# Optimization experiments

Hardware: AMD Instinct MI355X
Metric: run time of the kernel (lower is better)

The kernel has to match this reference:

```python
import jax, jax.numpy as jnp
import numpy as np

B, S, E, H = 2, 2048, 1024, 16
D = E // H  # head_dim = 64


def setup_inputs() -> dict:
    key = jax.random.key(0)
    ks = jax.random.split(key, 6)
    scale = 1.0 / np.sqrt(E)
    query = jax.random.normal(ks[0], (B, S, E), dtype=jnp.float32)
    key_t = jax.random.normal(ks[1], (B, S, E), dtype=jnp.float32)
    # causal mask: True where future positions should be masked
    attention_mask = jnp.triu(jnp.ones((S, S), dtype=jnp.bool_), k=1)
    wq = jax.random.normal(ks[2], (E, E), dtype=jnp.float32) * scale
    wk = jax.random.normal(ks[3], (E, E), dtype=jnp.float32) * scale
    wv = jax.random.normal(ks[4], (E, E), dtype=jnp.float32) * scale
    wo = jax.random.normal(ks[5], (E, E), dtype=jnp.float32) * scale
    return {"query": query, "key": key_t, "attention_mask": attention_mask,
            "wq": wq, "wk": wk, "wv": wv, "wo": wo}


def _split_heads(x):
    # (B, S, E) -> (B, H, S, D)
    return x.reshape(B, S, H, D).transpose(0, 2, 1, 3)


def reference(query, key, attention_mask, wq, wk, wv, wo):
    # self-attention (encoder_decoder_attention=False): k, v from query
    q = _split_heads(query @ wq.T)
    k = _split_heads(query @ wk.T)
    v = _split_heads(query @ wv.T)
    scores = jnp.einsum('bhqd,bhkd->bhqk', q, k) / np.sqrt(D)
    # causal mask broadcast (1,1,S,S)
    scores = jnp.where(attention_mask[None, None, :, :], -jnp.inf, scores)
    attn_weights = jax.nn.softmax(scores, axis=-1)
    # drop_out = 0.0, so dropout is identity
    attn_out = jnp.einsum('bhqk,bhkd->bhqd', attn_weights, v)
    attn_out = attn_out.transpose(0, 2, 1, 3).reshape(B, S, E)
    attn_out = attn_out @ wo.T
    return attn_out, attn_weights
```

## Files before the change

kernel.cpp:

```cpp
#include <hip/hip_runtime.h>
#include <hip/hip_bf16.h>
#include <cstdint>

#define S_LEN 2048
#define EMB 1024
#define NHEAD 16
#define HDIM 64
#define NB 2
#define MTOT (NB * S_LEN)

typedef __attribute__((ext_vector_type(8))) __bf16 bf16x8;
typedef __attribute__((ext_vector_type(8))) unsigned short us8;
typedef __attribute__((ext_vector_type(4))) unsigned short us4;
typedef __attribute__((ext_vector_type(4))) float f32x4;

__device__ __forceinline__ unsigned short f2b(float f) {
  unsigned int u = __float_as_uint(f);
  u = (u + 0x7FFFu + ((u >> 16) & 1u)) >> 16;
  return (unsigned short)u;
}
__device__ __forceinline__ unsigned short f2b_tr(float f) {
  return (unsigned short)(__float_as_uint(f) >> 16);
}
__device__ __forceinline__ float b2f(unsigned short u) {
  return __uint_as_float((unsigned int)u << 16);
}
__device__ __forceinline__ bf16x8 ld8(const unsigned short* p) {
  return __builtin_bit_cast(bf16x8, *(const us8*)p);
}
__device__ __forceinline__ void gload16(const void* g, void* l) {
  __builtin_amdgcn_global_load_lds(
      (const __attribute__((address_space(1))) unsigned int*)g,
      (__attribute__((address_space(3))) unsigned int*)l, 16, 0, 0);
}
__device__ __forceinline__ void st_nt(float* p, f32x4 v) {
  __builtin_nontemporal_store(v, (f32x4*)p);
}
__device__ __forceinline__ void bar_lds() {
  asm volatile("s_waitcnt lgkmcnt(0)" ::: "memory");
  __builtin_amdgcn_sched_barrier(0);
  __builtin_amdgcn_s_barrier();
}
__device__ __forceinline__ void fence_lds_wave() {
  asm volatile("s_waitcnt lgkmcnt(0)" ::: "memory");
  __builtin_amdgcn_sched_barrier(0);
}

__global__ void conv_fused(const float* __restrict__ X,
                           const float* __restrict__ wq, const float* __restrict__ wk,
                           const float* __restrict__ wv, const float* __restrict__ wo,
                           unsigned short* __restrict__ xb,
                           unsigned short* __restrict__ wb) {
  int i = blockIdx.x * blockDim.x + threadIdx.x;
  const float* s;
  unsigned short* o;
  int j;
  float sc = 1.0f;
  if (i < MTOT * EMB / 4) {
    s = X; j = i; o = xb;
  } else {
    int k = i - MTOT * EMB / 4;
    int sel = k >> 18;
    j = k & 262143;
    s = sel == 0 ? wq : sel == 1 ? wk : sel == 2 ? wv : wo;
    o = wb + (size_t)sel * EMB * EMB;
    if (sel == 0) sc = 0.125f;
  }
  float4 v = reinterpret_cast<const float4*>(s)[j];
  us4 ov;
  ov[0] = f2b(v.x * sc); ov[1] = f2b(v.y * sc);
  ov[2] = f2b(v.z * sc); ov[3] = f2b(v.w * sc);
  reinterpret_cast<us4*>(o)[j] = ov;
}

__global__ __launch_bounds__(256)
void vtrans(const unsigned short* __restrict__ V, unsigned short* __restrict__ VT) {
  __shared__ unsigned short Vs[64][72];
  const int s0 = blockIdx.x * 64;
  const int bh = blockIdx.y, b = bh >> 4, h = bh & 15;
  const unsigned short* Vb = V + (size_t)b * S_LEN * EMB + h * HDIM;
  const int t = threadIdx.x;
  {
    int row = t >> 2, c0 = (t & 3) * 16;
    const unsigned short* src = Vb + (size_t)(s0 + row) * EMB + c0;
    *(us8*)&Vs[row][c0] = *(const us8*)src;
    *(us8*)&Vs[row][c0 + 8] = *(const us8*)(src + 8);
  }
  __syncthreads();
  int d = t >> 2, sc = (t & 3) * 16;
  us8 o0, o1;
#pragma unroll
  for (int j = 0; j < 8; ++j) { o0[j] = Vs[sc + j][d]; o1[j] = Vs[sc + 8 + j][d]; }
  unsigned short* dst = VT + ((size_t)bh * HDIM + d) * S_LEN + s0 + sc;
  *(us8*)dst = o0;
  *(us8*)(dst + 8) = o1;
}

template <typename OT>
__global__ __launch_bounds__(256)
void gemm_bt(const unsigned short* __restrict__ A,
             const unsigned short* __restrict__ Wb,
             OT* __restrict__ Cb) {
  __shared__ unsigned short As[128 * 32];
  __shared__ unsigned short Bs[128 * 32];
  const int t = threadIdx.x;
  const int w = t >> 6, l = t & 63;
  const int m0 = blockIdx.x * 128;
  const int n0g = blockIdx.y * 128;
  const int wsel = n0g >> 10;
  const int n0 = n0g & 1023;
  const unsigned short* W = Wb + (size_t)wsel * ((size_t)EMB * EMB);
  OT* C = Cb + (size_t)wsel * ((size_t)MTOT * EMB);
  const int wr = (w >> 1) * 64, wc = (w & 1) * 64;
  const int fr = l & 15, fk = (l >> 4) * 8;
  const f32x4 fz = {0.f, 0.f, 0.f, 0.f};
  f32x4 acc[4][4];
  for (int i = 0; i < 4; i++)
    for (int j = 0; j < 4; j++) acc[i][j] = fz;
  const int srow = t >> 2, scol = (t & 3) * 8;
  const unsigned short* Ar = A + (size_t)(m0 + srow) * EMB + scol;
  const unsigned short* Wr = W + (size_t)(n0 + srow) * EMB + scol;
  unsigned short* lA = &As[t * 8];
  unsigned short* lB = &Bs[t * 8];
  for (int k0 = 0; k0 < EMB; k0 += 32) {
    gload16(Ar + k0, lA);
    gload16(Ar + (size_t)64 * EMB + k0, lA + 64 * 32);
    gload16(Wr + k0, lB);
    gload16(Wr + (size_t)64 * EMB + k0, lB + 64 * 32);
    __syncthreads();
    bf16x8 af[4], bg[4];
#pragma unroll
    for (int i = 0; i < 4; i++) {
      af[i] = ld8(&As[(wr + i * 16 + fr) * 32 + fk]);
      bg[i] = ld8(&Bs[(wc + i * 16 + fr) * 32 + fk]);
    }
#pragma unroll
    for (int i = 0; i < 4; i++)
#pragma unroll
      for (int j = 0; j < 4; j++)
        acc[i][j] = __builtin_amdgcn_mfma_f32_16x16x32_bf16(af[i], bg[j], acc[i][j], 0, 0, 0);
    __syncthreads();
  }
  const int cr = (l >> 4) * 4, cc = l & 15;
#pragma unroll
  for (int i = 0; i < 4; i++)
#pragma unroll
    for (int j = 0; j < 4; j++) {
      int m = m0 + wr + i * 16 + cr;
      int n = n0 + wc + j * 16 + cc;
      OT* dst = C + (size_t)m * EMB + n;
#pragma unroll
      for (int r = 0; r < 4; r++) {
        if constexpr (sizeof(OT) == 2)
          dst[(size_t)r * EMB] = f2b(acc[i][j][r]);
        else
          __builtin_nontemporal_store(acc[i][j][r], dst + (size_t)r * EMB);
      }
    }
}

__global__ __launch_bounds__(256, 3)
void attn_fwd(const unsigned short* __restrict__ Q,
              const unsigned short* __restrict__ K,
              const unsigned short* __restrict__ VT,
              unsigned short* __restrict__ AO,
              float* __restrict__ WT) {
  __shared__ __align__(16) unsigned char smem[9216 * 4];
  unsigned short* Ks  = (unsigned short*)smem;
  unsigned short* Vt  = (unsigned short*)(smem + 9216);
  unsigned short* PsA = (unsigned short*)(smem + 18432);
  unsigned short* PsB = (unsigned short*)(smem + 27648);
  unsigned short* QsA = PsA;
  unsigned short* QsB = PsB;
  unsigned short* OlA = PsA;
  unsigned short* OlB = PsB;

  const int t = threadIdx.x, w = t >> 6, l = t & 63;
  const int bh = blockIdx.x, b = bh >> 4, h = bh & 15;
  const int p = blockIdx.y;
  const int qA = p, qB = (S_LEN / 64 - 1) - p;
  const int ntA = qA + 1, ntB = qB + 1;
  const unsigned short* Qb = Q + (size_t)b * S_LEN * EMB + h * HDIM;
  const unsigned short* Kb = K + (size_t)b * S_LEN * EMB + h * HDIM;
  const unsigned short* VTb = VT + (size_t)bh * HDIM * S_LEN;
  const int fr = l & 15, fk = (l >> 4) * 8;
  const int rg = (l >> 4) * 4;
  const int qrowA = qA * 64 + w * 16 + rg;
  const int qrowB = qB * 64 + w * 16 + rg;
  const f32x4 fz = {0.f, 0.f, 0.f, 0.f};
  const int srow = t >> 3, scol = (t & 7) * 8;
  const int zrow = l >> 4, zcol = (l & 15) * 4;

  {
    int row = t >> 2, c0 = (t & 3) * 16;
    const unsigned short* sA = Qb + (size_t)(qA * 64 + row) * EMB + c0;
    const unsigned short* sB = Qb + (size_t)(qB * 64 + row) * EMB + c0;
    *(us8*)&QsA[row * 72 + c0] = *(const us8*)sA;
    *(us8*)&QsA[row * 72 + c0 + 8] = *(const us8*)(sA + 8);
    *(us8*)&QsB[row * 72 + c0] = *(const us8*)sB;
    *(us8*)&QsB[row * 72 + c0 + 8] = *(const us8*)(sB + 8);
  }
  __syncthreads();
  bf16x8 qaA0 = ld8(&QsA[(w * 16 + fr) * 72 + fk]);
  bf16x8 qaA1 = ld8(&QsA[(w * 16 + fr) * 72 + 32 + fk]);
  bf16x8 qaB0 = ld8(&QsB[(w * 16 + fr) * 72 + fk]);
  bf16x8 qaB1 = ld8(&QsB[(w * 16 + fr) * 72 + 32 + fk]);

  float lrA[4], lrB[4];
#pragma unroll
  for (int r = 0; r < 4; r++) { lrA[r] = 0.f; lrB[r] = 0.f; }

  us8 k0r = *(const us8*)(Kb + (size_t)srow * EMB + scol);
  us8 k1r = *(const us8*)(Kb + (size_t)(srow + 32) * EMB + scol);
  for (int it = 0; it < ntB; ++it) {
    *(us8*)&Ks[srow * 72 + scol] = k0r;
    *(us8*)&Ks[(srow + 32) * 72 + scol] = k1r;
    us8 k0n, k1n;
    if (it + 1 < ntB) {
      const unsigned short* kn = Kb + (size_t)((it + 1) * 64) * EMB;
      k0n = *(const us8*)(kn + (size_t)srow * EMB + scol);
      k1n = *(const us8*)(kn + (size_t)(srow + 32) * EMB + scol);
    }
    bar_lds();
    const int kc = it * 64;
    const bool doA = (it < ntA);
    const bool diagA = (it == ntA - 1), diagB = (it == ntB - 1);
#pragma unroll
    for (int c = 0; c < 4; ++c) {
      bf16x8 kb0 = ld8(&Ks[(c * 16 + fr) * 72 + fk]);
      bf16x8 kb1 = ld8(&Ks[(c * 16 + fr) * 72 + 32 + fk]);
      int ki = kc + c * 16 + fr;
      if (doA) {
        f32x4 dd = fz;
        dd = __builtin_amdgcn_mfma_f32_16x16x32_bf16(qaA0, kb0, dd, 0, 0, 0);
        dd = __builtin_amdgcn_mfma_f32_16x16x32_bf16(qaA1, kb1, dd, 0, 0, 0);
#pragma unroll
        for (int r = 0; r < 4; ++r) {
          float e = __expf(dd[r]);
          if (diagA && ki > qrowA + r) e = 0.f;
          lrA[r] += e;
        }
      }
      {
        f32x4 dd = fz;
        dd = __builtin_amdgcn_mfma_f32_16x16x32_bf16(qaB0, kb0, dd, 0, 0, 0);
        dd = __builtin_amdgcn_mfma_f32_16x16x32_bf16(qaB1, kb1, dd, 0, 0, 0);
#pragma unroll
        for (int r = 0; r < 4; ++r) {
          float e = __expf(dd[r]);
          if (diagB && ki > qrowB + r) e = 0.f;
          lrB[r] += e;
        }
      }
    }
    if (!doA) {
#pragma unroll
      for (int s4 = 0; s4 < 4; ++s4) {
        int rowl = s4 * 4 + zrow;
        st_nt(&WT[((size_t)bh * S_LEN + qA * 64 + w * 16 + rowl) * S_LEN + kc + zcol], fz);
      }
    }
    bar_lds();
    k0r = k0n; k1r = k1n;
  }
  for (int it = ntB; it < 32; ++it) {
    const int kc = it * 64;
#pragma unroll
    for (int s4 = 0; s4 < 4; ++s4) {
      int rowl = s4 * 4 + zrow;
      size_t rbase = (size_t)bh * S_LEN;
      st_nt(&WT[(rbase + qA * 64 + w * 16 + rowl) * S_LEN + kc + zcol], fz);
      st_nt(&WT[(rbase + qB * 64 + w * 16 + rowl) * S_LEN + kc + zcol], fz);
    }
  }
#pragma unroll
  for (int r = 0; r < 4; ++r) {
    float lA = lrA[r], lB = lrB[r];
    for (int s = 1; s < 16; s <<= 1) {
      lA += __shfl_xor(lA, s, 64);
      lB += __shfl_xor(lB, s, 64);
    }
    lrA[r] = 1.0f / lA;
    lrB[r] = 1.0f / lB;
  }

  f32x4 accA[4], accB[4];
#pragma unroll
  for (int i = 0; i < 4; i++) { accA[i] = fz; accB[i] = fz; }
  unsigned short* PsAw = PsA + w * (16 * 72);
  unsigned short* PsBw = PsB + w * (16 * 72);
  us8 v0r, v1r;
  k0r = *(const us8*)(Kb + (size_t)srow * EMB + scol);
  k1r = *(const us8*)(Kb + (size_t)(srow + 32) * EMB + scol);
  v0r = *(const us8*)(VTb + (size_t)srow * S_LEN + scol);
  v1r = *(const us8*)(VTb + (size_t)(srow + 32) * S_LEN + scol);
  for (int it = 0; it < ntB; ++it) {
    *(us8*)&Ks[srow * 72 + scol] = k0r;
    *(us8*)&Ks[(srow + 32) * 72 + scol] = k1r;
    *(us8*)&Vt[srow * 72 + scol] = v0r;
    *(us8*)&Vt[(srow + 32) * 72 + scol] = v1r;
    us8 k0n, k1n, v0n, v1n;
    if (it + 1 < ntB) {
      const int kc1 = (it + 1) * 64;
      const unsigned short* kn = Kb + (size_t)kc1 * EMB;
      k0n = *(const us8*)(kn + (size_t)srow * EMB + scol);
      k1n = *(const us8*)(kn + (size_t)(srow + 32) * EMB + scol);
      v0n = *(const us8*)(VTb + (size_t)srow * S_LEN + kc1 + scol);
      v1n = *(const us8*)(VTb + (size_t)(srow + 32) * S_LEN + kc1 + scol);
    }
    bar_lds();
    const int kc = it * 64;
    const bool doA = (it < ntA);
    const bool diagA = (it == ntA - 1), diagB = (it == ntB - 1);
#pragma unroll
    for (int c = 0; c < 4; ++c) {
      bf16x8 kb0 = ld8(&Ks[(c * 16 + fr) * 72 + fk]);
      bf16x8 kb1 = ld8(&Ks[(c * 16 + fr) * 72 + 32 + fk]);
      int ki = kc + c * 16 + fr;
      if (doA) {
        f32x4 dd = fz;
        dd = __builtin_amdgcn_mfma_f32_16x16x32_bf16(qaA0, kb0, dd, 0, 0, 0);
        dd = __builtin_amdgcn_mfma_f32_16x16x32_bf16(qaA1, kb1, dd, 0, 0, 0);
#pragma unroll
        for (int r = 0; r < 4; ++r) {
          float e = __expf(dd[r]);
          if (diagA && ki > qrowA + r) e = 0.f;
          PsAw[(rg + r) * 72 + c * 16 + fr] = f2b_tr(e * lrA[r]);
        }
      }
      {
        f32x4 dd = fz;
        dd = __builtin_amdgcn_mfma_f32_16x16x32_bf16(qaB0, kb0, dd, 0, 0, 0);
        dd = __builtin_amdgcn_mfma_f32_16x16x32_bf16(qaB1, kb1, dd, 0, 0, 0);
#pragma unroll
        for (int r = 0; r < 4; ++r) {
          float e = __expf(dd[r]);
          if (diagB && ki > qrowB + r) e = 0.f;
          PsBw[(rg + r) * 72 + c * 16 + fr] = f2b_tr(e * lrB[r]);
        }
      }
    }
    fence_lds_wave();
#pragma unroll
    for (int ks = 0; ks < 2; ++ks) {
      bf16x8 paA, paB;
      if (doA) paA = ld8(&PsAw[fr * 72 + ks * 32 + fk]);
      paB = ld8(&PsBw[fr * 72 + ks * 32 + fk]);
#pragma unroll
      for (int dt = 0; dt < 4; ++dt) {
        bf16x8 vb = ld8(&Vt[(dt * 16 + fr) * 72 + ks * 32 + fk]);
        if (doA) accA[dt] = __builtin_amdgcn_mfma_f32_16x16x32_bf16(paA, vb, accA[dt], 0, 0, 0);
        accB[dt] = __builtin_amdgcn_mfma_f32_16x16x32_bf16(paB, vb, accB[dt], 0, 0, 0);
      }
    }
    if (doA) {
#pragma unroll
      for (int s4 = 0; s4 < 4; ++s4) {
        int rowl = s4 * 4 + zrow;
        us4 pv = *(const us4*)&PsAw[rowl * 72 + zcol];
        f32x4 v;
#pragma unroll
        for (int j = 0; j < 4; ++j) v[j] = b2f(pv[j]);
        st_nt(&WT[((size_t)bh * S_LEN + qA * 64 + w * 16 + rowl) * S_LEN + kc + zcol], v);
      }
    }
#pragma unroll
    for (int s4 = 0; s4 < 4; ++s4) {
      int rowl = s4 * 4 + zrow;
      us4 pv = *(const us4*)&PsBw[rowl * 72 + zcol];
      f32x4 v;
#pragma unroll
      for (int j = 0; j < 4; ++j) v[j] = b2f(pv[j]);
      st_nt(&WT[((size_t)bh * S_LEN + qB * 64 + w * 16 + rowl) * S_LEN + kc + zcol], v);
    }
    bar_lds();
    k0r = k0n; k1r = k1n; v0r = v0n; v1r = v1n;
  }

#pragma unroll
  for (int dt = 0; dt < 4; ++dt)
#pragma unroll
    for (int r = 0; r < 4; ++r) {
      OlA[(w * 16 + rg + r) * 72 + dt * 16 + fr] = f2b(accA[dt][r]);
      OlB[(w * 16 + rg + r) * 72 + dt * 16 + fr] = f2b(accB[dt][r]);
    }
  __syncthreads();
  {
    int rowl = l >> 2, d0 = (l & 3) * 16;
    us8 a0 = *(const us8*)&OlA[(w * 16 + rowl) * 72 + d0];
    us8 a1 = *(const us8*)&OlA[(w * 16 + rowl) * 72 + d0 + 8];
    unsigned short* dA = AO + (size_t)(b * S_LEN + qA * 64 + w * 16 + rowl) * EMB + h * HDIM + d0;
    *(us8*)dA = a0;
    *(us8*)(dA + 8) = a1;
    us8 b0 = *(const us8*)&OlB[(w * 16 + rowl) * 72 + d0];
    us8 b1 = *(const us8*)&OlB[(w * 16 + rowl) * 72 + d0 + 8];
    unsigned short* dB = AO + (size_t)(b * S_LEN + qB * 64 + w * 16 + rowl) * EMB + h * HDIM + d0;
    *(us8*)dB = b0;
    *(us8*)(dB + 8) = b1;
  }
}

extern "C" void kernel_launch(void* const* d_in, const int* in_sizes, int n_in,
                              void* d_out, int out_size, void* d_ws, size_t ws_size,
                              hipStream_t stream) {
  const float* query = (const float*)d_in[0];
  const float* wq = (const float*)d_in[3];
  const float* wk = (const float*)d_in[4];
  const float* wv = (const float*)d_in[5];
  const float* wo = (const float*)d_in[6];

  float* out0 = (float*)d_out;
  float* wout = out0 + (size_t)MTOT * EMB;

  unsigned short* xb  = (unsigned short*)d_ws;
  unsigned short* wqb = xb + (size_t)MTOT * EMB;
  unsigned short* wob = wqb + (size_t)3 * EMB * EMB;
  unsigned short* qb  = wqb + (size_t)4 * EMB * EMB;
  unsigned short* kb  = qb + (size_t)MTOT * EMB;
  unsigned short* vb  = kb + (size_t)MTOT * EMB;
  unsigned short* ab  = vb + (size_t)MTOT * EMB;
  unsigned short* vtg = xb;

  conv_fused<<<dim3(8192), dim3(256), 0, stream>>>(query, wq, wk, wv, wo, xb, wqb);

  gemm_bt<unsigned short><<<dim3(MTOT / 128, 24), dim3(256), 0, stream>>>(xb, wqb, qb);

  vtrans<<<dim3(S_LEN / 64, NB * NHEAD), dim3(256), 0, stream>>>(vb, vtg);

  attn_fwd<<<dim3(NB * NHEAD, S_LEN / 128), dim3(256), 0, stream>>>(qb, kb, vtg, ab, wout);

  gemm_bt<float><<<dim3(MTOT / 128, 8), dim3(256), 0, stream>>>(ab, wob, out0);
}
```

Measured before the change: 226.8 us.

## Split attention work so each wave owns one query tile half, doubling grid

Each block now handles 32 query rows from tile A and 32 from tile B. Waves 0-1 handle tile A and waves 2-3 handle tile B, instead of every wave computing both tiles. The grid doubles with a z dimension, LDS shrinks from 36 KiB to 27 KiB, and launch bounds rise to 4 blocks per CU, all to raise occupancy and cut per-thread register pressure from the dual accumulators. In exchange, each K/V tile loaded into LDS now serves only 32 rows per tile, so K/V traffic doubles. Waves for the short tile also idle while the long-tile waves iterate.

Result: slower. 245.7 us (+8.3%).

```diff
diff --git a/kernel.cpp b/kernel.cpp
--- a/kernel.cpp
+++ b/kernel.cpp
@@ -159,56 +159,53 @@
     }
 }
 
-__global__ __launch_bounds__(256, 3)
+__global__ __launch_bounds__(256, 4)
 void attn_fwd(const unsigned short* __restrict__ Q,
               const unsigned short* __restrict__ K,
               const unsigned short* __restrict__ VT,
               unsigned short* __restrict__ AO,
               float* __restrict__ WT) {
-  __shared__ __align__(16) unsigned char smem[9216 * 4];
+  __shared__ __align__(16) unsigned char smem[27648];
   unsigned short* Ks  = (unsigned short*)smem;
   unsigned short* Vt  = (unsigned short*)(smem + 9216);
   unsigned short* PsA = (unsigned short*)(smem + 18432);
-  unsigned short* PsB = (unsigned short*)(smem + 27648);
-  unsigned short* QsA = PsA;
-  unsigned short* QsB = PsB;
-  unsigned short* OlA = PsA;
-  unsigned short* OlB = PsB;
+  unsigned short* PsB = (unsigned short*)(smem + 23040);
 
   const int t = threadIdx.x, w = t >> 6, l = t & 63;
-  const int bh = blockIdx.x, b = bh >> 4, h = bh & 15;
-  const int p = blockIdx.y;
-  const int qA = p, qB = (S_LEN / 64 - 1) - p;
-  const int ntA = qA + 1, ntB = qB + 1;
+  const int p = blockIdx.x;
+  const int bh = blockIdx.y, b = bh >> 4, h = bh & 15;
+  const int z = blockIdx.z;
+  const int qA = p, qB = 31 - p;
+  const int ntA = p + 1, ntB = 32 - p;
+  const int half = w >> 1;
+  const int wrow = (w & 1) * 16;
+  const int nt = half ? ntB : ntA;
+  const int qbase = (half ? qB : qA) * 64 + z * 32;
   const unsigned short* Qb = Q + (size_t)b * S_LEN * EMB + h * HDIM;
   const unsigned short* Kb = K + (size_t)b * S_LEN * EMB + h * HDIM;
   const unsigned short* VTb = VT + (size_t)bh * HDIM * S_LEN;
   const int fr = l & 15, fk = (l >> 4) * 8;
   const int rg = (l >> 4) * 4;
-  const int qrowA = qA * 64 + w * 16 + rg;
-  const int qrowB = qB * 64 + w * 16 + rg;
+  const int qrow = qbase + wrow + rg;
   const f32x4 fz = {0.f, 0.f, 0.f, 0.f};
   const int srow = t >> 3, scol = (t & 7) * 8;
   const int zrow = l >> 4, zcol = (l & 15) * 4;
+  unsigned short* Psh = half ? PsB : PsA;
 
   {
-    int row = t >> 2, c0 = (t & 3) * 16;
-    const unsigned short* sA = Qb + (size_t)(qA * 64 + row) * EMB + c0;
-    const unsigned short* sB = Qb + (size_t)(qB * 64 + row) * EMB + c0;
-    *(us8*)&QsA[row * 72 + c0] = *(const us8*)sA;
-    *(us8*)&QsA[row * 72 + c0 + 8] = *(const us8*)(sA + 8);
-    *(us8*)&QsB[row * 72 + c0] = *(const us8*)sB;
-    *(us8*)&QsB[row * 72 + c0 + 8] = *(const us8*)(sB + 8);
+    int row = t >> 3, c0 = (t & 7) * 8;
+    *(us8*)&PsA[row * 72 + c0] =
+        *(const us8*)(Qb + (size_t)(qA * 64 + z * 32 + row) * EMB + c0);
+    *(us8*)&PsB[row * 72 + c0] =
+        *(const us8*)(Qb + (size_t)(qB * 64 + z * 32 + row) * EMB + c0);
   }
   __syncthreads();
-  bf16x8 qaA0 = ld8(&QsA[(w * 16 + fr) * 72 + fk]);
-  bf16x8 qaA1 = ld8(&QsA[(w * 16 + fr) * 72 + 32 + fk]);
-  bf16x8 qaB0 = ld8(&QsB[(w * 16 + fr) * 72 + fk]);
-  bf16x8 qaB1 = ld8(&QsB[(w * 16 + fr) * 72 + 32 + fk]);
-
-  float lrA[4], lrB[4];
-#pragma unroll
-  for (int r = 0; r < 4; r++) { lrA[r] = 0.f; lrB[r] = 0.f; }
+  bf16x8 qa0 = ld8(&Psh[(wrow + fr) * 72 + fk]);
+  bf16x8 qa1 = ld8(&Psh[(wrow + fr) * 72 + 32 + fk]);
+
+  float lr[4];
+#pragma unroll
+  for (int r = 0; r < 4; r++) lr[r] = 0.f;
 
   us8 k0r = *(const us8*)(Kb + (size_t)srow * EMB + scol);
   us8 k1r = *(const us8*)(Kb + (size_t)(srow + 32) * EMB + scol);
@@ -223,41 +220,28 @@
     }
     bar_lds();
     const int kc = it * 64;
-    const bool doA = (it < ntA);
-    const bool diagA = (it == ntA - 1), diagB = (it == ntB - 1);
-#pragma unroll
-    for (int c = 0; c < 4; ++c) {
-      bf16x8 kb0 = ld8(&Ks[(c * 16 + fr) * 72 + fk]);
-      bf16x8 kb1 = ld8(&Ks[(c * 16 + fr) * 72 + 32 + fk]);
-      int ki = kc + c * 16 + fr;
-      if (doA) {
+    if (it < nt) {
+      const bool diag = (it == nt - 1);
+#pragma unroll
+      for (int c = 0; c < 4; ++c) {
+        bf16x8 kb0 = ld8(&Ks[(c * 16 + fr) * 72 + fk]);
+        bf16x8 kb1 = ld8(&Ks[(c * 16 + fr) * 72 + 32 + fk]);
         f32x4 dd = fz;
-        dd = __builtin_amdgcn_mfma_f32_16x16x32_bf16(qaA0, kb0, dd, 0, 0, 0);
-        dd = __builtin_amdgcn_mfma_f32_16x16x32_bf16(qaA1, kb1, dd, 0, 0, 0);
+        dd = __builtin_amdgcn_mfma_f32_16x16x32_bf16(qa0, kb0, dd, 0, 0, 0);
+        dd = __builtin_amdgcn_mfma_f32_16x16x32_bf16(qa1, kb1, dd, 0, 0, 0);
+        int ki = kc + c * 16 + fr;
 #pragma unroll
         for (int r = 0; r < 4; ++r) {
           float e = __expf(dd[r]);
-          if (diagA && ki > qrowA + r) e = 0.f;
-          lrA[r] += e;
+          if (diag && ki > qrow + r) e = 0.f;
+          lr[r] += e;
         }
       }
-      {
-        f32x4 dd = fz;
-        dd = __builtin_amdgcn_mfma_f32_16x16x32_bf16(qaB0, kb0, dd, 0, 0, 0);
-        dd = __builtin_amdgcn_mfma_f32_16x16x32_bf16(qaB1, kb1, dd, 0, 0, 0);
-#pragma unroll
-        for (int r = 0; r < 4; ++r) {
-          float e = __expf(dd[r]);
-          if (diagB && ki > qrowB + r) e = 0.f;
-          lrB[r] += e;
-        }
-      }
-    }
-    if (!doA) {
+    } else {
 #pragma unroll
       for (int s4 = 0; s4 < 4; ++s4) {
         int rowl = s4 * 4 + zrow;
-        st_nt(&WT[((size_t)bh * S_LEN + qA * 64 + w * 16 + rowl) * S_LEN + kc + zcol], fz);
+        st_nt(&WT[((size_t)bh * S_LEN + qbase + wrow + rowl) * S_LEN + kc + zcol], fz);
       }
     }
     bar_lds();
@@ -268,27 +252,19 @@
 #pragma unroll
     for (int s4 = 0; s4 < 4; ++s4) {
       int rowl = s4 * 4 + zrow;
-      size_t rbase = (size_t)bh * S_LEN;
-      st_nt(&WT[(rbase + qA * 64 + w * 16 + rowl) * S_LEN + kc + zcol], fz);
-      st_nt(&WT[(rbase + qB * 64 + w * 16 + rowl) * S_LEN + kc + zcol], fz);
+      st_nt(&WT[((size_t)bh * S_LEN + qbase + wrow + rowl) * S_LEN + kc + zcol], fz);
     }
   }
 #pragma unroll
   for (int r = 0; r < 4; ++r) {
-    float lA = lrA[r], lB = lrB[r];
-    for (int s = 1; s < 16; s <<= 1) {
-      lA += __shfl_xor(lA, s, 64);
-      lB += __shfl_xor(lB, s, 64);
-    }
-    lrA[r] = 1.0f / lA;
-    lrB[r] = 1.0f / lB;
-  }
-
-  f32x4 accA[4], accB[4];
-#pragma unroll
-  for (int i = 0; i < 4; i++) { accA[i] = fz; accB[i] = fz; }
-  unsigned short* PsAw = PsA + w * (16 * 72);
-  unsigned short* PsBw = PsB + w * (16 * 72);
+    float v = lr[r];
+    for (int s = 1; s < 16; s <<= 1) v += __shfl_xor(v, s, 64);
+    lr[r] = 1.0f / v;
+  }
+
+  f32x4 acc[4];
+#pragma unroll
+  for (int i = 0; i < 4; i++) acc[i] = fz;
   us8 v0r, v1r;
   k0r = *(const us8*)(Kb + (size_t)srow * EMB + scol);
   k1r = *(const us8*)(Kb + (size_t)(srow + 32) * EMB + scol);
@@ -310,68 +286,42 @@
     }
     bar_lds();
     const int kc = it * 64;
-    const bool doA = (it < ntA);
-    const bool diagA = (it == ntA - 1), diagB = (it == ntB - 1);
-#pragma unroll
-    for (int c = 0; c < 4; ++c) {
-      bf16x8 kb0 = ld8(&Ks[(c * 16 + fr) * 72 + fk]);
-      bf16x8 kb1 = ld8(&Ks[(c * 16 + fr) * 72 + 32 + fk]);
-      int ki = kc + c * 16 + fr;
-      if (doA) {
+    if (it < nt) {
+      const bool diag = (it == nt - 1);
+#pragma unroll
+      for (int c = 0; c < 4; ++c) {
+        bf16x8 kb0 = ld8(&Ks[(c * 16 + fr) * 72 + fk]);
+        bf16x8 kb1 = ld8(&Ks[(c * 16 + fr) * 72 + 32 + fk]);
         f32x4 dd = fz;
-        dd = __builtin_amdgcn_mfma_f32_16x16x32_bf16(qaA0, kb0, dd, 0, 0, 0);
-        dd = __builtin_amdgcn_mfma_f32_16x16x32_bf16(qaA1, kb1, dd, 0, 0, 0);
+        dd = __builtin_amdgcn_mfma_f32_16x16x32_bf16(qa0, kb0, dd, 0, 0, 0);
+        dd = __builtin_amdgcn_mfma_f32_16x16x32_bf16(qa1, kb1, dd, 0, 0, 0);
+        int ki = kc + c * 16 + fr;
 #pragma unroll
         for (int r = 0; r < 4; ++r) {
           float e = __expf(dd[r]);
-          if (diagA && ki > qrowA + r) e = 0.f;
-          PsAw[(rg + r) * 72 + c * 16 + fr] = f2b_tr(e * lrA[r]);
+          if (diag && ki > qrow + r) e = 0.f;
+          Psh[(wrow + rg + r) * 72 + c * 16 + fr] = f2b_tr(e * lr[r]);
         }
       }
-      {
-        f32x4 dd = fz;
-        dd = __builtin_amdgcn_mfma_f32_16x16x32_bf16(qaB0, kb0, dd, 0, 0, 0);
-        dd = __builtin_amdgcn_mfma_f32_16x16x32_bf16(qaB1, kb1, dd, 0, 0, 0);
-#pragma unroll
-        for (int r = 0; r < 4; ++r) {
-          float e = __expf(dd[r]);
-          if (diagB && ki > qrowB + r) e = 0.f;
-          PsBw[(rg + r) * 72 + c * 16 + fr] = f2b_tr(e * lrB[r]);
+      fence_lds_wave();
+#pragma unroll
+      for (int ks = 0; ks < 2; ++ks) {
+        bf16x8 pa = ld8(&Psh[(wrow + fr) * 72 + ks * 32 + fk]);
+#pragma unroll
+        for (int dt = 0; dt < 4; ++dt) {
+          bf16x8 vb = ld8(&Vt[(dt * 16 + fr) * 72 + ks * 32 + fk]);
+          acc[dt] = __builtin_amdgcn_mfma_f32_16x16x32_bf16(pa, vb, acc[dt], 0, 0, 0);
         }
       }
-    }
-    fence_lds_wave();
-#pragma unroll
-    for (int ks = 0; ks < 2; ++ks) {
-      bf16x8 paA, paB;
-      if (doA) paA = ld8(&PsAw[fr * 72 + ks * 32 + fk]);
-      paB = ld8(&PsBw[fr * 72 + ks * 32 + fk]);
-#pragma unroll
-      for (int dt = 0; dt < 4; ++dt) {
-        bf16x8 vb = ld8(&Vt[(dt * 16 + fr) * 72 + ks * 32 + fk]);
-        if (doA) accA[dt] = __builtin_amdgcn_mfma_f32_16x16x32_bf16(paA, vb, accA[dt], 0, 0, 0);
-        accB[dt] = __builtin_amdgcn_mfma_f32_16x16x32_bf16(paB, vb, accB[dt], 0, 0, 0);
-      }
-    }
-    if (doA) {
 #pragma unroll
       for (int s4 = 0; s4 < 4; ++s4) {
         int rowl = s4 * 4 + zrow;
-        us4 pv = *(const us4*)&PsAw[rowl * 72 + zcol];
+        us4 pv = *(const us4*)&Psh[(wrow + rowl) * 72 + zcol];
         f32x4 v;
 #pragma unroll
         for (int j = 0; j < 4; ++j) v[j] = b2f(pv[j]);
-        st_nt(&WT[((size_t)bh * S_LEN + qA * 64 + w * 16 + rowl) * S_LEN + kc + zcol], v);
-      }
-    }
-#pragma unroll
-    for (int s4 = 0; s4 < 4; ++s4) {
-      int rowl = s4 * 4 + zrow;
-      us4 pv = *(const us4*)&PsBw[rowl * 72 + zcol];
-      f32x4 v;
-#pragma unroll
-      for (int j = 0; j < 4; ++j) v[j] = b2f(pv[j]);
-      st_nt(&WT[((size_t)bh * S_LEN + qB * 64 + w * 16 + rowl) * S_LEN + kc + zcol], v);
+        st_nt(&WT[((size_t)bh * S_LEN + qbase + wrow + rowl) * S_LEN + kc + zcol], v);
+      }
     }
     bar_lds();
     k0r = k0n; k1r = k1n; v0r = v0n; v1r = v1n;
@@ -380,23 +330,21 @@
 #pragma unroll
   for (int dt = 0; dt < 4; ++dt)
 #pragma unroll
-    for (int r = 0; r < 4; ++r) {
-      OlA[(w * 16 + rg + r) * 72 + dt * 16 + fr] = f2b(accA[dt][r]);
-      OlB[(w * 16 + rg + r) * 72 + dt * 16 + fr] = f2b(accB[dt][r]);
-    }
+    for (int r = 0; r < 4; ++r)
+      Psh[(wrow + rg + r) * 72 + dt * 16 + fr] = f2b(acc[dt][r]);
   __syncthreads();
   {
-    int rowl = l >> 2, d0 = (l & 3) * 16;
-    us8 a0 = *(const us8*)&OlA[(w * 16 + rowl) * 72 + d0];
-    us8 a1 = *(const us8*)&OlA[(w * 16 + rowl) * 72 + d0 + 8];
-    unsigned short* dA = AO + (size_t)(b * S_LEN + qA * 64 + w * 16 + rowl) * EMB + h * HDIM + d0;
-    *(us8*)dA = a0;
-    *(us8*)(dA + 8) = a1;
-    us8 b0 = *(const us8*)&OlB[(w * 16 + rowl) * 72 + d0];
-    us8 b1 = *(const us8*)&OlB[(w * 16 + rowl) * 72 + d0 + 8];
-    unsigned short* dB = AO + (size_t)(b * S_LEN + qB * 64 + w * 16 + rowl) * EMB + h * HDIM + d0;
-    *(us8*)dB = b0;
-    *(us8*)(dB + 8) = b1;
+    int orow = t >> 2;
+    int oh = orow >> 5, orl = orow & 31;
+    int d0 = (t & 3) * 16;
+    const unsigned short* osrc =
+        (const unsigned short*)(smem + 18432 + oh * 4608) + orl * 72 + d0;
+    us8 o0 = *(const us8*)osrc;
+    us8 o1 = *(const us8*)(osrc + 8);
+    int grow = (oh ? qB : qA) * 64 + z * 32 + orl;
+    unsigned short* dst = AO + (size_t)(b * S_LEN + grow) * EMB + h * HDIM + d0;
+    *(us8*)dst = o0;
+    *(us8*)(dst + 8) = o1;
   }
 }
 
@@ -427,7 +375,7 @@
 
   vtrans<<<dim3(S_LEN / 64, NB * NHEAD), dim3(256), 0, stream>>>(vb, vtg);
 
-  attn_fwd<<<dim3(NB * NHEAD, S_LEN / 128), dim3(256), 0, stream>>>(qb, kb, vtg, ab, wout);
+  attn_fwd<<<dim3(16, NB * NHEAD, 2), dim3(256), 0, stream>>>(qb, kb, vtg, ab, wout);
 
   gemm_bt<float><<<dim3(MTOT / 128, 8), dim3(256), 0, stream>>>(ab, wob, out0);
 }
```
